# Performance work log

Hardware: AMD Instinct MI355X
Metric: run time of the kernel (lower is better)

Reference implementation:

```python
import jax, jax.numpy as jnp
import numpy as np
from jax.scipy.special import logsumexp

N_NODES = 20000
N_FEAT = 64
N_TPL = 10
TPL_NODES = 10
K_NEIGH = 15  # local neighborhood cap -> local graph size kloc = K+1 (self first)
N_EDGES = N_NODES * 16


def setup_inputs() -> dict:
    key = jax.random.key(0)
    k1, k2, k3, k4, k5 = jax.random.split(key, 5)
    x = jax.random.normal(k1, (N_NODES, N_FEAT), dtype=jnp.float32)
    edge_index = jax.random.randint(k2, (2, N_EDGES), 0, N_NODES, dtype=jnp.int32)
    # template_initialisation: randint{0,1} adjacency + N(0, 0.01) noise
    adj = jax.random.randint(k3, (N_TPL, TPL_NODES, TPL_NODES), 0, 2).astype(jnp.float32)
    templates = adj + 0.01 * jax.random.normal(k4, (N_TPL, TPL_NODES, TPL_NODES), dtype=jnp.float32)
    # template features ~ N(0.0012, 0.02)
    templates_features = 0.0012 + 0.02 * jax.random.normal(
        k5, (N_TPL, TPL_NODES, N_FEAT), dtype=jnp.float32)
    alpha0 = jnp.array([0.5], dtype=jnp.float32)
    return {"x": x, "edge_index": edge_index, "templates": templates,
            "templates_features": templates_features, "alpha0": alpha0}


def _fgw_distances(x, edge_index, templates, templates_features, alpha0,
                   K=K_NEIGH, n_outer=3, n_sink=5):
    """Per-node fused GW distance between the node's local (star) subgraph and
    each learned template, solved with an entropic proximal / Sinkhorn scheme.
    Returns [N, T]."""
    N, F = x.shape
    Tn, n, _ = templates.shape
    kloc = K + 1

    # ---- build fixed-size neighbor lists from edge_index (int ops, constant) ----
    src, dst = edge_index[0], edge_index[1]
    E = src.shape[0]
    order = jnp.argsort(src)
    src_s, dst_s = src[order], dst[order]
    deg = jnp.zeros((N,), jnp.int32).at[src].add(1)
    start = jnp.cumsum(deg) - deg                       # CSR row starts
    rank = jnp.arange(E, dtype=jnp.int32) - start[src_s]  # position within each node's list
    # rank >= K falls out of bounds -> dropped
    neigh = jnp.zeros((N, K), jnp.int32).at[src_s, rank].set(dst_s, mode="drop")
    nb_mask = (jnp.arange(K)[None, :] < jnp.minimum(deg, K)[:, None]).astype(x.dtype)  # [N,K]

    # ---- local graphs: self node first, then up to K neighbors ----
    xloc = jnp.concatenate([x[:, None, :], x[neigh]], axis=1)  # [N, kloc, F]
    m = jnp.concatenate([jnp.ones((N, 1), x.dtype), nb_mask], axis=1)  # [N, kloc]
    p = m / jnp.sum(m, -1, keepdims=True)                # node-side marginal
    q = jnp.full((n,), 1.0 / n, x.dtype)                 # template-side marginal

    # star adjacency of the 1-hop neighborhood
    row0 = jnp.concatenate([jnp.zeros((N, 1), x.dtype), nb_mask], axis=1)
    C1 = jnp.zeros((N, kloc, kloc), x.dtype).at[:, 0, :].set(row0).at[:, :, 0].set(row0)
    C2 = templates  # [T, n, n]

    # feature cost M[n_node, t, k, m] = ||xloc - y||^2
    M = (jnp.sum(xloc ** 2, -1)[:, None, :, None]
         + jnp.sum(templates_features ** 2, -1)[None, :, None, :]
         - 2.0 * jnp.einsum("nkf,tmf->ntkm", xloc, templates_features))

    alpha = jax.nn.sigmoid(alpha0)[0]

    # GW square-loss constant terms (Peyre et al. trick)
    hC1 = jnp.einsum("nkl,nl->nk", C1 ** 2, p)   # [N, kloc]
    hC2 = jnp.einsum("tmr,r->tm", C2 ** 2, q)    # [T, n]
    constC = hC1[:, None, :, None] + hC2[None, :, None, :]

    def gw_tens(Tp):  # Tp: [N, T, kloc, n]
        tmp = jnp.einsum("nkl,ntlm->ntkm", C1, Tp)
        return constC - 2.0 * jnp.einsum("ntkm,trm->ntkr", tmp, C2)

    eps = 0.05 * jax.lax.stop_gradient(jnp.mean(M)) + 1e-6
    logp = jnp.where(m > 0, jnp.log(jnp.maximum(p, 1e-30)), -1e9)[:, None, :]  # [N,1,kloc]
    logq = jnp.log(q)  # [n]

    Tp = p[:, None, :, None] * q[None, None, None, :]  # independent-coupling init
    f = jnp.zeros((N, Tn, kloc), x.dtype)
    g = jnp.zeros((N, Tn, n), x.dtype)
    for _ in range(n_outer):  # outer FGW linearization steps
        G = (1.0 - alpha) * M + 2.0 * alpha * gw_tens(Tp)
        logK = -G / eps
        for _ in range(n_sink):  # log-domain Sinkhorn on linearized cost
            f = eps * (logp - logsumexp(logK + g[:, :, None, :] / eps, axis=-1))
            g = eps * (logq - logsumexp(logK + f[:, :, :, None] / eps, axis=-2))
        Tp = jnp.exp(logK + f[:, :, :, None] / eps + g[:, :, None, :] / eps)

    dist = ((1.0 - alpha) * jnp.sum(M * Tp, axis=(-2, -1))
            + alpha * jnp.sum(gw_tens(Tp) * Tp, axis=(-2, -1)))
    return dist  # [N, T]


def reference(x, edge_index, templates, templates_features, alpha0):
    return _fgw_distances(x, edge_index, templates, templates_features, alpha0)
```

## Files before the change

### kernel.cpp

```cpp
#include <hip/hip_runtime.h>

#define N_NODES 20000
#define NPAIRS  10000
#define N_EDGES 320000
#define CAP     48
#define KN      15
#define GRID_MAIN 2500

typedef _Float16 half_t;
typedef _Float16 half2_t __attribute__((ext_vector_type(2)));
typedef float f32x2 __attribute__((ext_vector_type(2)));

#define P_ALPHA 0
#define P_BETA  1
#define P_IEPS2 2
#define P_EPS   3
#define P_HC2   16
#define P_RSC2  216
#define P_F1    316

#define OFF_CNT    0u
#define OFF_S2X    80000u
#define OFF_STATS  160000u
#define OFF_FLAG   160520u
#define OFF_PAD    160524u
#define OFF_NBC    160528u
#define OFF_NEIGH  240528u
#define OFF_BUF    1440528u
#define OFF_WCT    5280528u
#define OFF_PARAMS 6560528u
#define MEMSET_LEN 160528u

#define TF_STRIDE 648

template<int CTRL>
__device__ __forceinline__ float dpp_add(float v) {
  int s = __builtin_bit_cast(int, v);
  int r = __builtin_amdgcn_update_dpp(0, s, CTRL, 0xF, 0xF, true);
  return v + __builtin_bit_cast(float, r);
}
__device__ __forceinline__ float sum16(float v) {
  v = dpp_add<0x128>(v);
  v = dpp_add<0x124>(v);
  v = dpp_add<0x122>(v);
  v = dpp_add<0x121>(v);
  return v;
}
__device__ __forceinline__ float bcast16(float v) {
  return __builtin_bit_cast(float,
      __builtin_amdgcn_ds_swizzle(__builtin_bit_cast(int, v), 0x010));
}
__device__ __forceinline__ float fdot2(half2_t a, half2_t b, float c) {
  return __builtin_amdgcn_fdot2(a, b, c, false);
}
__device__ __forceinline__ half2_t h2(unsigned int u) {
  return __builtin_bit_cast(half2_t, u);
}
__device__ __forceinline__ float sgpr(float v) {
  return __builtin_bit_cast(float,
      __builtin_amdgcn_readfirstlane(__builtin_bit_cast(int, v)));
}
__device__ __forceinline__ f32x2 pk_fma(f32x2 a, f32x2 b, f32x2 c) {
  f32x2 d;
  asm("v_pk_fma_f32 %0, %1, %2, %3" : "=v"(d) : "v"(a), "v"(b), "v"(c));
  return d;
}
__device__ __forceinline__ f32x2 pk_mul(f32x2 a, f32x2 b) {
  f32x2 d;
  asm("v_pk_mul_f32 %0, %1, %2" : "=v"(d) : "v"(a), "v"(b));
  return d;
}

__global__ void k_scatter(const int* __restrict__ ei, int* __restrict__ cnt,
                          int* __restrict__ buf) {
  int e = blockIdx.x * blockDim.x + threadIdx.x;
  if (e >= N_EDGES) return;
  int s = ei[e];
  int slot = atomicAdd(&cnt[s], 1);
  if (slot < CAP) buf[s * CAP + slot] = e;
}

#define SS_BLOCKS 1250
__global__ void __launch_bounds__(256)
k_sel(const int* __restrict__ ei, const int* __restrict__ cnt,
      const int* __restrict__ buf, int* __restrict__ nbc_g,
      int* __restrict__ neigh, int* __restrict__ wct,
      int* __restrict__ padc) {
  const int lane = threadIdx.x & 63;
  const int wid = threadIdx.x >> 6;
  const int* dst = ei + N_EDGES;
  __shared__ int padsh;
  if (threadIdx.x == 0) padsh = 0;
  __syncthreads();
  int padacc = 0;

  for (int w = blockIdx.x * 4 + wid; w < N_NODES; w += SS_BLOCKS * 4) {
    int c = cnt[w];
    int cc = c < CAP ? c : CAP;
    int e = (lane < cc) ? buf[w * CAP + lane] : 0x7fffffff;
    int nb = c < KN ? c : KN;
    bool sel;
    if (cc <= KN) {
      sel = lane < cc;
    } else {
      int rank = 0;
      for (int j = 0; j < cc; j++) {
        int ej = __shfl(e, j);
        rank += (ej < e) ? 1 : 0;
      }
      sel = (e != 0x7fffffff) && (rank < KN);
    }
    unsigned long long mask = __ballot(sel);
    if (sel) {
      int pos = __popcll(mask & ((1ull << lane) - 1ull));
      int d = dst[e];
      neigh[w * KN + pos] = d;
      atomicAdd(&wct[d], 1);
    }
    if (lane == 0) { nbc_g[w] = nb; padacc += KN - nb; }
  }
  if (lane == 0 && padacc) atomicAdd(&padsh, padacc);
  __syncthreads();
  if (threadIdx.x == 0 && padsh) atomicAdd(padc, padsh);
}

#define PB 200
__global__ void __launch_bounds__(256)
k_pass(const float* __restrict__ x, half_t* __restrict__ xh,
       const int* __restrict__ wct, const int* __restrict__ padc,
       float* __restrict__ s2xh, double* __restrict__ stats,
       int* __restrict__ flag, const float* __restrict__ tf,
       const float* __restrict__ c2, const float* __restrict__ alpha0,
       float* __restrict__ params) {
  const int lane = threadIdx.x & 63;
  const int wid = threadIdx.x >> 6;
  const int tid = threadIdx.x;
  const int pad = *padc;
  float accx = 0.f, acc2 = 0.f;

  for (int n = blockIdx.x * 4 + wid; n < N_NODES; n += PB * 4) {
    float xv = x[n * 64 + lane];
    half_t hv = (half_t)xv;
    xh[n * 64 + lane] = hv;
    float hf = (float)hv;
    float sq = hf * hf;
#pragma unroll
    for (int off = 32; off > 0; off >>= 1) sq += __shfl_xor(sq, off, 64);
    if (lane == 0) s2xh[n] = sq;
    float wt = (float)(1 + wct[n] + ((n == 0) ? pad : 0));
    accx = fmaf(wt, xv, accx);
    acc2 = fmaf(wt, xv * xv, acc2);
  }

#pragma unroll
  for (int off = 32; off > 0; off >>= 1) acc2 += __shfl_xor(acc2, off, 64);
  __shared__ float redx[4][64];
  __shared__ float red2[4];
  __shared__ int lastsh;
  redx[wid][lane] = accx;
  if (lane == 0) red2[wid] = acc2;
  __syncthreads();
  if (tid < 64) {
    float s = redx[0][tid] + redx[1][tid] + redx[2][tid] + redx[3][tid];
    atomicAdd(&stats[1 + tid], (double)s);
  }
  if (tid == 0)
    atomicAdd(&stats[0], (double)(red2[0] + red2[1] + red2[2] + red2[3]));
  __syncthreads();
  if (tid == 0) {
    __threadfence();
    int old = atomicAdd(flag, 1);
    lastsh = (old == PB - 1) ? 1 : 0;
  }
  __syncthreads();
  if (!lastsh) return;
  __threadfence();
  __shared__ float sh[4];
  if (tid < 64) {
    float s = 0.f, s2 = 0.f;
    for (int tm = 0; tm < 100; tm++) { float v = tf[tm * 64 + tid]; s += v; s2 += v * v; }
    double inv16N = 1.0 / (double)(N_NODES * 16);
    double cross = (stats[1 + tid] * inv16N) * ((double)s / 100.0);
    double B = (double)s2 / 100.0;
    double term = B - 2.0 * cross;
#pragma unroll
    for (int off = 32; off > 0; off >>= 1) term += __shfl_xor(term, off, 64);
    if (tid == 0) {
      double A = stats[0] * inv16N;
      double meanM = A + term;
      float eps = (float)(0.05 * meanM) + 1e-6f;
      float a0 = alpha0[0];
      float alpha = 1.f / (1.f + expf(-a0));
      params[P_ALPHA] = alpha;
      params[P_BETA]  = 1.f - alpha;
      params[P_IEPS2] = 1.4426950408889634f / eps;
      params[P_EPS]   = eps;
      sh[0] = alpha; sh[1] = 1.f - alpha; sh[2] = 1.4426950408889634f / eps;
    }
  }
  __syncthreads();
  if (tid < 100) {
    float alpha = sh[0], beta = sh[1], ieps2 = sh[2];
    int t = tid / 10, mm = tid % 10;
    float h = 0.f;
    for (int r = 0; r < 10; r++) { float cv = c2[t * 100 + mm * 10 + r]; h += cv * cv; }
    float hc2v = 0.1f * h;
    params[P_HC2 + tid] = hc2v;
    float s2 = 0.f;
    for (int f = 0; f < 64; f++) { float v = tf[tid * 64 + f]; s2 += v * v; }
    float rs = 0.f;
    for (int m2_ = 0; m2_ < 10; m2_++) rs += c2[t * 100 + mm * 10 + m2_];
    params[P_RSC2 + tid] = rs;
    params[P_F1 + tid] = (beta * s2 + 2.0f * alpha * hc2v) * (-ieps2);
  }
}

__global__ void __launch_bounds__(320, 6)
k_main(const half_t* __restrict__ xh, const float* __restrict__ tf_g,
       const float* __restrict__ c2_g, const int* __restrict__ nbc_g,
       const int* __restrict__ neigh_g, const float* __restrict__ params,
       const float* __restrict__ s2x_g, float* __restrict__ out) {
  __shared__ __align__(16) half_t tf_l[10 * TF_STRIDE];
  __shared__ __align__(16) float c2_l[1000];
  __shared__ __align__(16) float hc2_l[100];
  __shared__ __align__(16) float rsc2_l[100];
  __shared__ __align__(16) float F1_l[100];
  __shared__ __align__(16) float bsb_l[20][10][2];

  const int tid = threadIdx.x;
  const int node_s = tid / 160;
  const int s = tid % 160;
  const int t = s >> 4;
  const int k = s & 15;
  const bool k0 = (k == 0);
  const int grp = node_s * 10 + t;

  for (int i = tid; i < 6400; i += 320) {
    int tt = i / 640, rem = i - tt * 640;
    tf_l[tt * TF_STRIDE + rem] = (half_t)tf_g[i];
  }
  for (int i = tid; i < 1000; i += 320) c2_l[i] = c2_g[i];
  if (tid < 100) {
    hc2_l[tid]  = params[P_HC2 + tid];
    rsc2_l[tid] = params[P_RSC2 + tid];
    F1_l[tid]   = params[P_F1 + tid];
  }

  const float alpha = sgpr(params[P_ALPHA]);
  const float beta  = sgpr(params[P_BETA]);
  const float ieps2 = sgpr(params[P_IEPS2]);
  const float eps   = sgpr(params[P_EPS]);
  const float niep  = -ieps2;
  const float twoal = 2.0f * alpha;
  const float ctv10 = 0.2f * twoal * ieps2;
  const float cab   = 2.0f * beta * ieps2;
  const float c_a2d = -eps * 0.69314718056f;
  const float twoal01 = 0.1f * twoal;
  const f32x2 cab2 = {cab, cab};
  const f32x2 ctv2 = {ctv10, ctv10};

  const int idx_c2 = t * 100 + ((k < 10) ? k : 9) * 10;
  __syncthreads();

  const int kk = (k == 0) ? 0 : (k - 1);
  const half_t* tfb = &tf_l[t * TF_STRIDE];
  int p = blockIdx.x;
  int nb_pf = nbc_g[2 * p + node_s];
  int nbr_pf = neigh_g[(2 * p + node_s) * KN + kk];

#pragma unroll 1
  for (; p < NPAIRS; p += gridDim.x) {
    const int v = 2 * p + node_s;
    const int nb = nb_pf;
    const int srcn = (k == 0) ? v : (kk < nb ? nbr_pf : 0);
    const float s2x = s2x_g[srcn];
    const uint4* xr = (const uint4*)(xh + (size_t)srcn * 64);

    uint4 q[8];
#pragma unroll
    for (int r = 0; r < 8; r++) q[r] = xr[r];

    {
      int vn = 2 * (p + gridDim.x) + node_s;
      vn = vn < N_NODES ? vn : 0;
      nb_pf = nbc_g[vn];
      nbr_pf = neigh_g[vn * KN + kk];
    }

    float acc[10];
#pragma unroll
    for (int m = 0; m < 10; m++) {
      float a = 0.0f;
#pragma unroll
      for (int ch = 0; ch < 4; ch++) {
        uint4 tqa = *(const uint4*)&tfb[m * 64 + ch * 16];
        uint4 tqb = *(const uint4*)&tfb[m * 64 + ch * 16 + 8];
        const uint4 qa = q[2 * ch];
        const uint4 qb = q[2 * ch + 1];
        a = fdot2(h2(tqa.x), h2(qa.x), a);
        a = fdot2(h2(tqa.y), h2(qa.y), a);
        a = fdot2(h2(tqa.z), h2(qa.z), a);
        a = fdot2(h2(tqa.w), h2(qa.w), a);
        a = fdot2(h2(tqb.x), h2(qb.x), a);
        a = fdot2(h2(tqb.y), h2(qb.y), a);
        a = fdot2(h2(tqb.z), h2(qb.z), a);
        a = fdot2(h2(tqb.w), h2(qb.w), a);
      }
      acc[m] = a;
    }

    const float inv = 1.0f / (float)(1 + nb);
    const float pk = (k <= nb) ? inv : 0.0f;
    const float hC1k = (k == 0) ? (float)nb * inv : ((k <= nb) ? inv : 0.0f);
    const float base = (beta * s2x + twoal * hC1k) * niep;
    const float ctm  = ctv10 * ((k == 0) ? (float)nb * inv : inv);
    const f32x2 base2 = {base, base};
    const f32x2 ctm2 = {ctm, ctm};

    f32x2 Ab2[5];
#pragma unroll
    for (int j = 0; j < 5; j++) {
      f32x2 f1v = *(const f32x2*)&F1_l[t * 10 + 2 * j];
      f32x2 av = {acc[2 * j], acc[2 * j + 1]};
      Ab2[j] = pk_fma(cab2, av, f1v + base2);
    }

    f32x2 K2[5], vv2[5];
    float u = 1.0f;
#pragma unroll
    for (int j = 0; j < 5; j++) { vv2[j][0] = 1.0f; vv2[j][1] = 1.0f; }

#pragma unroll
    for (int j = 0; j < 5; j++) {
      f32x2 rs = *(const f32x2*)&rsc2_l[t * 10 + 2 * j];
      f32x2 arg = pk_fma(ctm2, rs, Ab2[j]);
      f32x2 Kv;
      Kv[0] = __builtin_amdgcn_exp2f(arg[0]);
      Kv[1] = __builtin_amdgcn_exp2f(arg[1]);
      K2[j] = Kv;
    }

#pragma unroll 1
    for (int o = 0; o < 3; o++) {
#pragma unroll 1
      for (int it = 0; it < 5; it++) {
        f32x2 kv = {0.0f, 0.0f};
#pragma unroll
        for (int j = 0; j < 5; j++) kv = pk_fma(K2[j], vv2[j], kv);
        u = pk * __builtin_amdgcn_rcpf(kv[0] + kv[1]);
        f32x2 up = {u, u};
#pragma unroll
        for (int j = 0; j < 5; j++) {
          f32x2 Ku = pk_mul(K2[j], up);
          f32x2 nv;
          nv[0] = __builtin_amdgcn_rcpf(sum16(Ku[0]));
          nv[1] = __builtin_amdgcn_rcpf(sum16(Ku[1]));
          vv2[j] = nv;
        }
      }
      if (o == 2) break;
      {
        const f32x2 up = {u, u};
        float B = 0.0f, SB = 0.0f;
#pragma unroll
        for (int j = 0; j < 5; j++) {
          float2 c2p = *(const float2*)&c2_l[idx_c2 + 2 * j];
          f32x2 tk2 = pk_mul(pk_mul(K2[j], vv2[j]), up);
          B  = fmaf(bcast16(tk2[0]), c2p.x, B);
          SB = fmaf(sum16(tk2[0]),   c2p.x, SB);
          B  = fmaf(bcast16(tk2[1]), c2p.y, B);
          SB = fmaf(sum16(tk2[1]),   c2p.y, SB);
        }
        if (k < 10) { bsb_l[grp][k][0] = B; bsb_l[grp][k][1] = SB; }
        __threadfence_block();
#pragma unroll
        for (int j = 0; j < 5; j++) {
          float4 bv = *(const float4*)&bsb_l[grp][2 * j][0];
          f32x2 tv2;
          tv2[0] = k0 ? (bv.y - bv.x) : bv.x;
          tv2[1] = k0 ? (bv.w - bv.z) : bv.z;
          f32x2 arg = pk_fma(ctv2, tv2, Ab2[j]);
          f32x2 Kv;
          Kv[0] = __builtin_amdgcn_exp2f(arg[0]);
          Kv[1] = __builtin_amdgcn_exp2f(arg[1]);
          K2[j] = Kv;
        }
        __threadfence_block();
      }
    }

    {
      const f32x2 up = {u, u};
      f32x2 tkf[5];
      float B = 0.0f, SB = 0.0f;
#pragma unroll
      for (int j = 0; j < 5; j++) {
        float2 c2p = *(const float2*)&c2_l[idx_c2 + 2 * j];
        tkf[j] = pk_mul(pk_mul(K2[j], vv2[j]), up);
        B  = fmaf(bcast16(tkf[j][0]), c2p.x, B);
        SB = fmaf(sum16(tkf[j][0]),   c2p.x, SB);
        B  = fmaf(bcast16(tkf[j][1]), c2p.y, B);
        SB = fmaf(sum16(tkf[j][1]),   c2p.y, SB);
      }
      if (k < 10) { bsb_l[grp][k][0] = B; bsb_l[grp][k][1] = SB; }
      __threadfence_block();
      float dd = 0.0f;
#pragma unroll
      for (int j = 0; j < 5; j++) {
        float4 bv = *(const float4*)&bsb_l[grp][2 * j][0];
        float2 h2v = *(const float2*)&hc2_l[t * 10 + 2 * j];
        float tva = k0 ? (bv.y - bv.x) : bv.x;
        float tvb = k0 ? (bv.w - bv.z) : bv.z;
        float c1a = fmaf(alpha, hC1k + h2v.x, twoal01 * tva);
        float c1b = fmaf(alpha, hC1k + h2v.y, twoal01 * tvb);
        float coa = fmaf(c_a2d, Ab2[j][0], -c1a);
        float cob = fmaf(c_a2d, Ab2[j][1], -c1b);
        dd = fmaf(coa, tkf[j][0], dd);
        dd = fmaf(cob, tkf[j][1], dd);
      }
      __threadfence_block();
      dd = sum16(dd * 0.1f);
      if (k == 0) out[v * 10 + t] = dd;
    }
  }
}

extern "C" void kernel_launch(void* const* d_in, const int* in_sizes, int n_in,
                              void* d_out, int out_size, void* d_ws, size_t ws_size,
                              hipStream_t stream) {
  const float* x  = (const float*)d_in[0];
  const int*   ei = (const int*)d_in[1];
  const float* c2 = (const float*)d_in[2];
  const float* tf = (const float*)d_in[3];
  const float* a0 = (const float*)d_in[4];
  float* out = (float*)d_out;
  char* ws = (char*)d_ws;
  int*    cnt    = (int*)(ws + OFF_CNT);
  float*  s2xh   = (float*)(ws + OFF_S2X);
  double* stats  = (double*)(ws + OFF_STATS);
  int*    flag   = (int*)(ws + OFF_FLAG);
  int*    padc   = (int*)(ws + OFF_PAD);
  int*    nbc    = (int*)(ws + OFF_NBC);
  int*    neigh  = (int*)(ws + OFF_NEIGH);
  int*    buf    = (int*)(ws + OFF_BUF);
  half_t* xhalf  = (half_t*)(ws + OFF_BUF);
  int*    wct    = (int*)(ws + OFF_WCT);
  float*  params = (float*)(ws + OFF_PARAMS);
  (void)in_sizes; (void)n_in; (void)out_size; (void)ws_size;

  hipMemsetAsync(ws, 0, MEMSET_LEN, stream);
  hipMemsetAsync(ws + OFF_WCT, 0, 80000, stream);
  k_scatter<<<N_EDGES / 256, 256, 0, stream>>>(ei, cnt, buf);
  k_sel<<<SS_BLOCKS, 256, 0, stream>>>(ei, cnt, buf, nbc, neigh, wct, padc);
  k_pass<<<PB, 256, 0, stream>>>(x, xhalf, wct, padc, s2xh, stats, flag,
                                 tf, c2, a0, params);
  k_main<<<GRID_MAIN, 320, 0, stream>>>(xhalf, tf, c2, nbc, neigh, params, s2xh, out);
}
```

Measured before the change: 369.6 us.

## Software-pipeline next pair's feature loads and merge workspace memsets

The main loop now prefetches the next iteration's neighbor index, s2x value and full half-precision feature row into registers while the current pair's Sinkhorn work runs, instead of loading them at the top of each iteration. It also raises wave priority during the compute phase, and moves the wct counter buffer next to the other zeroed regions so a single memset covers it. This aims to hide global-memory latency and remove one memset launch, at the cost of extra VGPRs that could lower occupancy.

```diff
diff --git a/kernel.cpp b/kernel.cpp
--- a/kernel.cpp
+++ b/kernel.cpp
@@ -20,16 +20,16 @@
 #define P_F1    316
 
 #define OFF_CNT    0u
-#define OFF_S2X    80000u
+#define OFF_WCT    80000u
 #define OFF_STATS  160000u
 #define OFF_FLAG   160520u
 #define OFF_PAD    160524u
+#define MEMSET_LEN 160528u
 #define OFF_NBC    160528u
-#define OFF_NEIGH  240528u
-#define OFF_BUF    1440528u
-#define OFF_WCT    5280528u
-#define OFF_PARAMS 6560528u
-#define MEMSET_LEN 160528u
+#define OFF_S2X    240528u
+#define OFF_NEIGH  320528u
+#define OFF_BUF    1520528u
+#define OFF_PARAMS 5360528u
 
 #define TF_STRIDE 648
 
@@ -264,28 +264,32 @@
 
   const int kk = (k == 0) ? 0 : (k - 1);
   const half_t* tfb = &tf_l[t * TF_STRIDE];
+
   int p = blockIdx.x;
-  int nb_pf = nbc_g[2 * p + node_s];
-  int nbr_pf = neigh_g[(2 * p + node_s) * KN + kk];
+  int nb_c, s2i_c;
+  float s2x_c;
+  uint4 q[8];
+  {
+    const int v0 = 2 * p + node_s;
+    nb_c = nbc_g[v0];
+    int nbr = neigh_g[v0 * KN + kk];
+    s2i_c = k0 ? v0 : (kk < nb_c ? nbr : 0);
+    s2x_c = s2x_g[s2i_c];
+    const uint4* xr = (const uint4*)(xh + (size_t)s2i_c * 64);
+#pragma unroll
+    for (int r = 0; r < 8; r++) q[r] = xr[r];
+  }
 
 #pragma unroll 1
   for (; p < NPAIRS; p += gridDim.x) {
     const int v = 2 * p + node_s;
-    const int nb = nb_pf;
-    const int srcn = (k == 0) ? v : (kk < nb ? nbr_pf : 0);
-    const float s2x = s2x_g[srcn];
-    const uint4* xr = (const uint4*)(xh + (size_t)srcn * 64);
-
-    uint4 q[8];
-#pragma unroll
-    for (int r = 0; r < 8; r++) q[r] = xr[r];
-
-    {
-      int vn = 2 * (p + gridDim.x) + node_s;
-      vn = vn < N_NODES ? vn : 0;
-      nb_pf = nbc_g[vn];
-      nbr_pf = neigh_g[vn * KN + kk];
-    }
+    const int nb = nb_c;
+    const float s2x = s2x_c;
+
+    int vn = 2 * (p + gridDim.x) + node_s;
+    vn = vn < N_NODES ? vn : 0;
+    int nb_n = nbc_g[vn];
+    int nbr_n = neigh_g[vn * KN + kk];
 
     float acc[10];
 #pragma unroll
@@ -309,6 +313,17 @@
       acc[m] = a;
     }
 
+    int s2i_n = k0 ? vn : (kk < nb_n ? nbr_n : 0);
+    float s2x_n = s2x_g[s2i_n];
+    uint4 qn0, qn1, qn2, qn3, qn4, qn5, qn6, qn7;
+    {
+      const uint4* xrn = (const uint4*)(xh + (size_t)s2i_n * 64);
+      qn0 = xrn[0]; qn1 = xrn[1]; qn2 = xrn[2]; qn3 = xrn[3];
+      qn4 = xrn[4]; qn5 = xrn[5]; qn6 = xrn[6]; qn7 = xrn[7];
+    }
+
+    __builtin_amdgcn_s_setprio(1);
+
     const float inv = 1.0f / (float)(1 + nb);
     const float pk = (k <= nb) ? inv : 0.0f;
     const float hC1k = (k == 0) ? (float)nb * inv : ((k <= nb) ? inv : 0.0f);
@@ -422,6 +437,12 @@
       dd = sum16(dd * 0.1f);
       if (k == 0) out[v * 10 + t] = dd;
     }
+
+    __builtin_amdgcn_s_setprio(0);
+
+    nb_c = nb_n; s2x_c = s2x_n; s2i_c = s2i_n;
+    q[0] = qn0; q[1] = qn1; q[2] = qn2; q[3] = qn3;
+    q[4] = qn4; q[5] = qn5; q[6] = qn6; q[7] = qn7;
   }
 }
 
@@ -436,20 +457,19 @@
   float* out = (float*)d_out;
   char* ws = (char*)d_ws;
   int*    cnt    = (int*)(ws + OFF_CNT);
-  float*  s2xh   = (float*)(ws + OFF_S2X);
+  int*    wct    = (int*)(ws + OFF_WCT);
   double* stats  = (double*)(ws + OFF_STATS);
   int*    flag   = (int*)(ws + OFF_FLAG);
   int*    padc   = (int*)(ws + OFF_PAD);
   int*    nbc    = (int*)(ws + OFF_NBC);
+  float*  s2xh   = (float*)(ws + OFF_S2X);
   int*    neigh  = (int*)(ws + OFF_NEIGH);
   int*    buf    = (int*)(ws + OFF_BUF);
   half_t* xhalf  = (half_t*)(ws + OFF_BUF);
-  int*    wct    = (int*)(ws + OFF_WCT);
   float*  params = (float*)(ws + OFF_PARAMS);
   (void)in_sizes; (void)n_in; (void)out_size; (void)ws_size;
 
   hipMemsetAsync(ws, 0, MEMSET_LEN, stream);
-  hipMemsetAsync(ws + OFF_WCT, 0, 80000, stream);
   k_scatter<<<N_EDGES / 256, 256, 0, stream>>>(ei, cnt, buf);
   k_sel<<<SS_BLOCKS, 256, 0, stream>>>(ei, cnt, buf, nbc, neigh, wct, padc);
   k_pass<<<PB, 256, 0, stream>>>(x, xhalf, wct, padc, s2xh, stats, flag,
```

Result: slower. 403.1 us (+9.1%).
